# Optimization experiments

Measured on AMD Instinct MI355X. Metric: run time of the kernel, lower is better.

Reference implementation:

```python
import jax, jax.numpy as jnp
import numpy as np

INPUT_SIZE = 32768
MINICOL_SIZE = 8
NUM_MINICOLS = INPUT_SIZE // MINICOL_SIZE  # 4096
SYN_PERM_CONNECTED = 0.1
NUM_ACTIVE = 82  # num_active_columns_per_inhibition_area


def setup_inputs() -> dict:
    key = jax.random.key(0)
    k1, k2 = jax.random.split(key)
    input_vector = (jax.random.uniform(k1, (INPUT_SIZE,)) < 0.05).astype(jnp.float32)
    # connections: rand binarized at syn_perm_connected, per initialize_connections().
    connections = (jax.random.uniform(k2, (NUM_MINICOLS, INPUT_SIZE)) >= SYN_PERM_CONNECTED
                   ).astype(jnp.float32)
    boosting_factors = jnp.ones((NUM_MINICOLS,), dtype=jnp.float32)
    return {"input_vector": input_vector, "connections": connections,
            "boosting_factors": boosting_factors}


def reference(input_vector, connections, boosting_factors):
    # compute_overlap: per-minicolumn masked sum == matvec over binary mask.
    overlap = jnp.einsum("ci,i->c", connections, input_vector)  # [C]
    boosted = overlap * boosting_factors                         # [C]
    # global_inhibition_func: top-k winners -> binary active-column SDR.
    _, winners = jax.lax.top_k(boosted, NUM_ACTIVE)
    active_columns = jnp.zeros((NUM_MINICOLS,), dtype=boosted.dtype).at[winners].set(1.0)
    # Return active mask and the masked boosted overlap (winner activations).
    return active_columns, active_columns * boosted
```

## Files before the change

### kernel.cpp

```cpp
#include <hip/hip_runtime.h>

#define INPUT_SIZE 32768
#define NUM_COLS   4096
#define NUM_ACTIVE 82
#define ROWS_PER_BLOCK 8
#define NF4 (INPUT_SIZE / 4)

typedef float v4f __attribute__((ext_vector_type(4)));

__device__ __forceinline__ float dot4(v4f a, v4f b) {
    return a.x * b.x + a.y * b.y + a.z * b.z + a.w * b.w;
}

__global__ __launch_bounds__(256) void matvec_boost_kernel(
    const float* __restrict__ conn, const float* __restrict__ input,
    const float* __restrict__ boost, float* __restrict__ overlap)
{
    const int r0 = blockIdx.x * ROWS_PER_BLOCK;
    const int t  = threadIdx.x;
    const v4f* in4 = (const v4f*)input;
    const v4f* row[ROWS_PER_BLOCK];
    #pragma unroll
    for (int r = 0; r < ROWS_PER_BLOCK; ++r)
        row[r] = (const v4f*)(conn + (size_t)(r0 + r) * INPUT_SIZE);

    float acc[ROWS_PER_BLOCK];
    #pragma unroll
    for (int r = 0; r < ROWS_PER_BLOCK; ++r) acc[r] = 0.f;

    for (int k = t; k < NF4; k += 512) {
        const int k2 = k + 256;
        v4f b0 = in4[k];
        v4f b1 = in4[k2];
        v4f a0[ROWS_PER_BLOCK], a1[ROWS_PER_BLOCK];
        #pragma unroll
        for (int r = 0; r < ROWS_PER_BLOCK; ++r) {
            a0[r] = __builtin_nontemporal_load(&row[r][k]);
            a1[r] = __builtin_nontemporal_load(&row[r][k2]);
        }
        #pragma unroll
        for (int r = 0; r < ROWS_PER_BLOCK; ++r)
            acc[r] += dot4(a0[r], b0) + dot4(a1[r], b1);
    }

    #pragma unroll
    for (int r = 0; r < ROWS_PER_BLOCK; ++r) {
        float a = acc[r];
        #pragma unroll
        for (int off = 32; off > 0; off >>= 1)
            a += __shfl_down(a, off, 64);
        acc[r] = a;
    }

    __shared__ float part[4][ROWS_PER_BLOCK];
    const int wave = t >> 6;
    if ((t & 63) == 0) {
        #pragma unroll
        for (int r = 0; r < ROWS_PER_BLOCK; ++r) part[wave][r] = acc[r];
    }
    __syncthreads();
    if (t < ROWS_PER_BLOCK) {
        float tot = part[0][t] + part[1][t] + part[2][t] + part[3][t];
        overlap[r0 + t] = tot * boost[r0 + t];
    }
}

__global__ __launch_bounds__(64) void topk_mask_kernel(
    const float* __restrict__ vals, float* __restrict__ out)
{
    const int c = blockIdx.x;
    const int lane = threadIdx.x;
    const float v = vals[c];
    const float4* v4 = (const float4*)vals;

    int cnt = 0;
    #pragma unroll
    for (int k = 0; k < NUM_COLS / 4 / 64; ++k) {
        const int i4 = lane + 64 * k;
        float4 b = v4[i4];
        const int j = i4 * 4;
        cnt += (b.x > v) || (b.x == v && (j + 0) < c);
        cnt += (b.y > v) || (b.y == v && (j + 1) < c);
        cnt += (b.z > v) || (b.z == v && (j + 2) < c);
        cnt += (b.w > v) || (b.w == v && (j + 3) < c);
    }
    #pragma unroll
    for (int off = 32; off > 0; off >>= 1)
        cnt += __shfl_down(cnt, off, 64);

    if (lane == 0) {
        const bool act = cnt < NUM_ACTIVE;
        out[c] = act ? 1.0f : 0.0f;
        out[NUM_COLS + c] = act ? v : 0.0f;
    }
}

extern "C" void kernel_launch(void* const* d_in, const int* in_sizes, int n_in,
                              void* d_out, int out_size, void* d_ws, size_t ws_size,
                              hipStream_t stream) {
    const float* input = (const float*)d_in[0];
    const float* conn  = (const float*)d_in[1];
    const float* boost = (const float*)d_in[2];
    float* out = (float*)d_out;
    float* ov  = (float*)d_ws;

    matvec_boost_kernel<<<NUM_COLS / ROWS_PER_BLOCK, 256, 0, stream>>>(conn, input, boost, ov);
    topk_mask_kernel<<<NUM_COLS, 64, 0, stream>>>(ov, out);
}
```

Before: 658.5 us.

## Compact sparse input nonzeros and gather only matching connection entries

```diff
diff --git a/kernel.cpp b/kernel.cpp
--- a/kernel.cpp
+++ b/kernel.cpp
@@ -4,43 +4,52 @@
 #define NUM_COLS   4096
 #define NUM_ACTIVE 82
 #define ROWS_PER_BLOCK 8
-#define NF4 (INPUT_SIZE / 4)
 
-typedef float v4f __attribute__((ext_vector_type(4)));
 
-__device__ __forceinline__ float dot4(v4f a, v4f b) {
-    return a.x * b.x + a.y * b.y + a.z * b.z + a.w * b.w;
+__global__ void zero_counter_kernel(int* __restrict__ cnt) {
+    if (threadIdx.x == 0) *cnt = 0;
 }
 
-__global__ __launch_bounds__(256) void matvec_boost_kernel(
-    const float* __restrict__ conn, const float* __restrict__ input,
+__global__ __launch_bounds__(256) void compact_kernel(
+    const float* __restrict__ input, int* __restrict__ nnz,
+    int* __restrict__ idx, float* __restrict__ val)
+{
+    const int gid  = blockIdx.x * 256 + threadIdx.x;
+    const int lane = threadIdx.x & 63;
+    const float v  = input[gid];
+    const unsigned long long m = __ballot(v != 0.0f);
+    const int nactive = __popcll(m);
+    const int myoff   = __popcll(m & ((1ull << lane) - 1ull));
+    int base = 0;
+    if (lane == 0 && nactive) base = atomicAdd(nnz, nactive);
+    base = __shfl(base, 0, 64);
+    if (v != 0.0f) { idx[base + myoff] = gid; val[base + myoff] = v; }
+}
+
+__global__ __launch_bounds__(256) void gather_matvec_kernel(
+    const float* __restrict__ conn, const int* __restrict__ nnzp,
+    const int* __restrict__ idx, const float* __restrict__ val,
     const float* __restrict__ boost, float* __restrict__ overlap)
 {
     const int r0 = blockIdx.x * ROWS_PER_BLOCK;
     const int t  = threadIdx.x;
-    const v4f* in4 = (const v4f*)input;
-    const v4f* row[ROWS_PER_BLOCK];
+    const int nnz = *nnzp;
+
+    const float* row[ROWS_PER_BLOCK];
     #pragma unroll
     for (int r = 0; r < ROWS_PER_BLOCK; ++r)
-        row[r] = (const v4f*)(conn + (size_t)(r0 + r) * INPUT_SIZE);
+        row[r] = conn + (size_t)(r0 + r) * INPUT_SIZE;
 
     float acc[ROWS_PER_BLOCK];
     #pragma unroll
     for (int r = 0; r < ROWS_PER_BLOCK; ++r) acc[r] = 0.f;
 
-    for (int k = t; k < NF4; k += 512) {
-        const int k2 = k + 256;
-        v4f b0 = in4[k];
-        v4f b1 = in4[k2];
-        v4f a0[ROWS_PER_BLOCK], a1[ROWS_PER_BLOCK];
-        #pragma unroll
-        for (int r = 0; r < ROWS_PER_BLOCK; ++r) {
-            a0[r] = __builtin_nontemporal_load(&row[r][k]);
-            a1[r] = __builtin_nontemporal_load(&row[r][k2]);
-        }
+    for (int j = t; j < nnz; j += 256) {
+        const int   ii = idx[j];
+        const float v  = val[j];
         #pragma unroll
         for (int r = 0; r < ROWS_PER_BLOCK; ++r)
-            acc[r] += dot4(a0[r], b0) + dot4(a1[r], b1);
+            acc[r] += row[r][ii] * v;
     }
 
     #pragma unroll
@@ -102,8 +111,14 @@
     const float* conn  = (const float*)d_in[1];
     const float* boost = (const float*)d_in[2];
     float* out = (float*)d_out;
+
     float* ov  = (float*)d_ws;
+    int*   nnz = (int*)(ov + NUM_COLS);
+    int*   idx = nnz + 64;
+    float* val = (float*)(idx + INPUT_SIZE);
 
-    matvec_boost_kernel<<<NUM_COLS / ROWS_PER_BLOCK, 256, 0, stream>>>(conn, input, boost, ov);
+    zero_counter_kernel<<<1, 64, 0, stream>>>(nnz);
+    compact_kernel<<<INPUT_SIZE / 256, 256, 0, stream>>>(input, nnz, idx, val);
+    gather_matvec_kernel<<<NUM_COLS / ROWS_PER_BLOCK, 256, 0, stream>>>(conn, nnz, idx, val, boost, ov);
     topk_mask_kernel<<<NUM_COLS, 64, 0, stream>>>(ov, out);
 }
```

Result: slower. 684.3 us (+3.9%).
